# Performance work log

Hardware: AMD Instinct MI355X
Metric: run time of the kernel (lower is better)

The kernel has to match this reference:

```python
import jax, jax.numpy as jnp
import numpy as np

N = 50000
E = 800000
D_IN = 128
D_HID = 128
D_OUT = 64
BN_EPS = 1e-5


def setup_inputs() -> dict:
    key = jax.random.key(0)
    ks = jax.random.split(key, 8)
    x = jax.random.normal(ks[0], (N, D_IN), dtype=jnp.float32)
    edge_index = jax.random.randint(ks[1], (2, E), 0, N, dtype=jnp.int64)
    # fc1
    W1 = jax.random.normal(ks[2], (D_IN, D_HID), dtype=jnp.float32) / np.sqrt(D_IN)
    b1 = jnp.zeros((D_HID,), dtype=jnp.float32)
    # bn1 affine params
    gamma = jnp.ones((D_HID,), dtype=jnp.float32)
    beta = jnp.zeros((D_HID,), dtype=jnp.float32)
    # fc2
    W2 = jax.random.normal(ks[3], (D_HID, D_OUT), dtype=jnp.float32) / np.sqrt(D_HID)
    b2 = jnp.zeros((D_OUT,), dtype=jnp.float32)
    return {"x": x, "W1": W1, "b1": b1, "gamma": gamma, "beta": beta,
            "W2": W2, "b2": b2, "edge_index": edge_index}


def _propagate(x, row, col):
    # add self loops for every node (reference convention)
    n = x.shape[0]
    sl = jnp.arange(n, dtype=row.dtype)
    row_f = jnp.concatenate([row, sl])
    col_f = jnp.concatenate([col, sl])
    # symmetric degree normalization: deg computed over destinations (col)
    deg = jax.ops.segment_sum(jnp.ones_like(col_f, dtype=x.dtype), col_f, num_segments=n)
    dis = deg ** -0.5
    w = dis[col_f] * dis[row_f]                       # [E+N]
    msg = w[:, None] * x[row_f]                       # [E+N, D] gather + scale
    return jax.ops.segment_sum(msg, col_f, num_segments=n)  # scatter-add


def reference(x, W1, b1, gamma, beta, W2, b2, edge_index):
    row, col = edge_index[0], edge_index[1]
    h = x @ W1 + b1                                   # [N, D_HID]
    h = _propagate(h, row, col)
    # BatchNorm1d with batch statistics (training-mode math, deterministic)
    mu = jnp.mean(h, axis=0)
    var = jnp.var(h, axis=0)
    h = (h - mu) * jax.lax.rsqrt(var + BN_EPS) * gamma + beta
    h = jax.nn.relu(h)
    # dropout treated as identity (eval) for a deterministic reference
    h = h @ W2 + b2                                   # [N, D_OUT]
    h = _propagate(h, row, col)
    return jax.nn.log_softmax(h, axis=1)
```

## Files before the change

### kernel.cpp

```cpp
#include <hip/hip_runtime.h>
#include <hip/hip_bf16.h>

#define N_NODES 50000
#define NE      800000
#define DIN     128
#define DHID    128
#define DOUT    64
#define BN_EPS  1e-5f
#define SLOT    64
#define NBUK    196
#define BCAP    4864
#define EPB     2048
#define NPART   32
#define LDW     132
#define LDW2    132
#define G1_BLOCKS ((N_NODES + 63) / 64)

typedef __hip_bfloat16 bf16;
typedef short bf16x8 __attribute__((ext_vector_type(8)));
typedef float f32x4 __attribute__((ext_vector_type(4)));

__device__ __forceinline__ float ldf(const void* p, int i, int isbf) {
    if (isbf) return __bfloat162float(((const bf16*)p)[i]);
    return ((const float*)p)[i];
}
__device__ __forceinline__ unsigned short f2b(float f) {
    bf16 h = __float2bfloat16(f);
    return *(unsigned short*)&h;
}
__device__ __forceinline__ float2 up2(unsigned int u) {
    return make_float2(__uint_as_float(u << 16), __uint_as_float(u & 0xffff0000u));
}
__device__ __forceinline__ unsigned int pk2(float a, float b) {
    return ((unsigned int)f2b(a)) | (((unsigned int)f2b(b)) << 16);
}

#define DETECT_ISBF(W1raw, tid, sdet, isbf_out)                                   \
    if ((tid) == 0) sdet = 0;                                                     \
    __syncthreads();                                                              \
    {                                                                             \
        unsigned int u_ = ((unsigned int)((const unsigned short*)(W1raw))[tid]) << 16; \
        float f_ = fabsf(__uint_as_float(u_));                                    \
        if (!isnan(f_) && !isinf(f_) && f_ > 1e4f) atomicOr(&sdet, 1);            \
    }                                                                             \
    __syncthreads();                                                              \
    const int isbf_out = !sdet;

__global__ __launch_bounds__(256) void k_binA(const void* eiraw, int* __restrict__ gcnt,
                                              unsigned int* __restrict__ bpk) {
    __shared__ int hist4[4][256];
    __shared__ int cur4[4][256];
    __shared__ int eofs[256], gbase[256];
    __shared__ int wsum[4];
    __shared__ unsigned int stg[EPB];
    __shared__ int sdet;
    int tid = threadIdx.x;
    int lane = tid & 63;
    int wv = tid >> 6;
    if (tid == 0) sdet = 0;
    #pragma unroll
    for (int w2 = 0; w2 < 4; ++w2) hist4[w2][tid] = 0;
    __syncthreads();
    if (tid < 64 && ((const unsigned int*)eiraw)[2 * tid + 1] != 0u) atomicOr(&sdet, 1);
    __syncthreads();
    const int isll = !sdet;

    int e0 = blockIdx.x * EPB;
    int nE = NE - e0; if (nE > EPB) nE = EPB;
    int r[8], c[8];
    #pragma unroll
    for (int q = 0; q < 8; ++q) {
        int li = q * 256 + tid;
        if (li < nE) {
            int e = e0 + li;
            if (isll) { r[q] = (int)((const long long*)eiraw)[e]; c[q] = (int)((const long long*)eiraw)[NE + e]; }
            else      { r[q] = ((const int*)eiraw)[e];            c[q] = ((const int*)eiraw)[NE + e]; }
            atomicAdd(&hist4[wv][c[q] >> 8], 1);
        } else r[q] = -1;
    }
    __syncthreads();
    int h0 = hist4[0][tid], h1 = hist4[1][tid], h2 = hist4[2][tid], h3 = hist4[3][tid];
    int tot = h0 + h1 + h2 + h3;
    int inc = tot;
    #pragma unroll
    for (int off = 1; off < 64; off <<= 1) {
        int u = __shfl_up(inc, off, 64);
        if (lane >= off) inc += u;
    }
    if (lane == 63) wsum[wv] = inc;
    __syncthreads();
    int woff = 0;
    #pragma unroll
    for (int w2 = 0; w2 < 3; ++w2) if (w2 < wv) woff += wsum[w2];
    int ex = woff + inc - tot;
    eofs[tid] = ex;
    cur4[0][tid] = ex;
    cur4[1][tid] = ex + h0;
    cur4[2][tid] = ex + h0 + h1;
    cur4[3][tid] = ex + h0 + h1 + h2;
    if (tid < NBUK) gbase[tid] = atomicAdd(&gcnt[tid], tot);
    __syncthreads();
    #pragma unroll
    for (int q = 0; q < 8; ++q) {
        if (r[q] >= 0) {
            int b = c[q] >> 8;
            int p = atomicAdd(&cur4[wv][b], 1);
            stg[p] = ((unsigned int)b << 24) | ((unsigned int)(c[q] & 255) << 16) | (unsigned int)r[q];
        }
    }
    __syncthreads();
    for (int i = tid; i < nE; i += 256) {
        unsigned int v = stg[i];
        int b = v >> 24;
        int pos = gbase[b] + (i - eofs[b]);
        if (pos < BCAP) bpk[(size_t)b * BCAP + pos] = v;
    }
}

__global__ __launch_bounds__(256) void k_binB_gemm1(const unsigned int* __restrict__ bpk,
                                                    const int* __restrict__ gcnt,
                                                    int* __restrict__ counts, float* __restrict__ disv,
                                                    int* __restrict__ ej,
                                                    const void* __restrict__ x, const void* __restrict__ W1,
                                                    const void* __restrict__ b1,
                                                    unsigned short* __restrict__ g1) {
    __shared__ __align__(16) char smraw[33792];
    __shared__ int sdet;
    int tid = threadIdx.x;

    if (blockIdx.x < NBUK) {
        int (*cnt4)[256] = (int(*)[256])smraw;
        int (*cur4)[256] = (int(*)[256])(smraw + 4096);
        int* eofs        = (int*)(smraw + 8192);
        int* wsum        = (int*)(smraw + 9216);
        unsigned int* stg = (unsigned int*)(smraw + 9232);

        int b = blockIdx.x;
        int lane = tid & 63;
        int wv = tid >> 6;
        int m = gcnt[b]; if (m > BCAP) m = BCAP;
        #pragma unroll
        for (int w2 = 0; w2 < 4; ++w2) cnt4[w2][tid] = 0;
        __syncthreads();
        const unsigned int* src = bpk + (size_t)b * BCAP;
        for (int i = tid; i < m; i += 256)
            atomicAdd(&cnt4[wv][(src[i] >> 16) & 255], 1);
        __syncthreads();
        int h0 = cnt4[0][tid], h1 = cnt4[1][tid], h2 = cnt4[2][tid], h3 = cnt4[3][tid];
        int hv = h0 + h1 + h2 + h3;
        int inc = hv;
        #pragma unroll
        for (int off = 1; off < 64; off <<= 1) {
            int u = __shfl_up(inc, off, 64);
            if (lane >= off) inc += u;
        }
        if (lane == 63) wsum[wv] = inc;
        __syncthreads();
        int woff = 0;
        #pragma unroll
        for (int w2 = 0; w2 < 3; ++w2) if (w2 < wv) woff += wsum[w2];
        int ex = woff + inc - hv;
        eofs[tid] = ex;
        cur4[0][tid] = ex;
        cur4[1][tid] = ex + h0;
        cur4[2][tid] = ex + h0 + h1;
        cur4[3][tid] = ex + h0 + h1 + h2;
        int c0 = b << 8;
        int cg = c0 + tid;
        if (cg < N_NODES) {
            counts[cg] = hv;
            disv[cg] = rsqrtf((float)(hv + 1));
            int hc = hv < SLOT ? hv : SLOT;
            int hp = (hc + 15) & ~15; if (hp > SLOT) hp = SLOT;
            for (int k = hc; k < hp; ++k) ej[(size_t)cg * SLOT + k] = N_NODES;
        } else if (cg == N_NODES) {
            disv[cg] = 0.f;
        }
        __syncthreads();
        for (int i = tid; i < m; i += 256) {
            unsigned int v = src[i];
            int cl = (v >> 16) & 255;
            int p = atomicAdd(&cur4[wv][cl], 1);
            stg[p] = v & 0x00ffffffu;
        }
        __syncthreads();
        for (int i = tid; i < m; i += 256) {
            unsigned int v = stg[i];
            int cl = v >> 16;
            int k = i - eofs[cl];
            if (k < SLOT) ej[(size_t)(c0 + cl) * SLOT + k] = (int)(v & 0xffffu);
        }
    } else {
        unsigned short* wt = (unsigned short*)smraw;
        DETECT_ISBF(W1, tid, sdet, isbf)

        #pragma unroll 4
        for (int i = 0; i < 64; ++i) {
            int idx = i * 256 + tid;
            int k = idx >> 7, n = idx & 127;
            wt[n * LDW + k] = isbf ? ((const unsigned short*)W1)[idx]
                                   : f2b(((const float*)W1)[idx]);
        }
        __syncthreads();

        int lane = tid & 63;
        int wave = tid >> 6;
        int bid = blockIdx.x - NBUK;
        int m0 = bid * 64 + wave * 16;
        int lm = lane & 15;
        int quad = lane >> 4;

        bf16x8 a[4];
        int arow = m0 + lm;
        int arow_c = arow < N_NODES ? arow : 0;
        if (isbf) {
            const unsigned short* xb = (const unsigned short*)x;
            #pragma unroll
            for (int q = 0; q < 4; ++q)
                a[q] = *(const bf16x8*)(xb + arow_c * DIN + q * 32 + quad * 8);
        } else {
            const float* xf = (const float*)x;
            #pragma unroll
            for (int q = 0; q < 4; ++q) {
                bf16x8 t;
                #pragma unroll
                for (int j = 0; j < 8; ++j)
                    t[j] = (short)f2b(xf[arow_c * DIN + q * 32 + quad * 8 + j]);
                a[q] = t;
            }
        }

        #pragma unroll
        for (int nt = 0; nt < 8; ++nt) {
            int n0 = nt * 16;
            f32x4 acc = {0.f, 0.f, 0.f, 0.f};
            #pragma unroll
            for (int q = 0; q < 4; ++q) {
                bf16x8 b = *(const bf16x8*)(wt + (n0 + lm) * LDW + q * 32 + quad * 8);
                acc = __builtin_amdgcn_mfma_f32_16x16x32_bf16(a[q], b, acc, 0, 0, 0);
            }
            float bias = ldf(b1, n0 + lm, isbf);
            #pragma unroll
            for (int r = 0; r < 4; ++r) {
                int grow = m0 + quad * 4 + r;
                if (grow <= N_NODES) {
                    float val = (grow < N_NODES) ? (acc[r] + bias) : 0.f;
                    g1[grow * DHID + n0 + lm] = f2b(val);
                }
            }
        }
    }
}

__global__ __launch_bounds__(256) void k_prop1(const int* __restrict__ counts, const float* __restrict__ disv,
                                               const int* __restrict__ ej,
                                               const unsigned int* __restrict__ g1p,
                                               unsigned int* __restrict__ agg1p,
                                               float* __restrict__ statsP) {
    __shared__ float sp[1024];
    int tid = threadIdx.x;
    int w = tid >> 6;
    int n = blockIdx.x * 4 + w;
    n = __builtin_amdgcn_readfirstlane(n);
    int lane = tid & 63;
    float ax = 0.f, ay = 0.f;
    if (n < N_NODES) {
        int cnt = counts[n];
        float dv = disv[n];
        int t = cnt < SLOT ? cnt : SLOT;
        int tp = (t + 15) & ~15; if (tp > SLOT) tp = SLOT;
        const int* ejn = ej + (size_t)n * SLOT;
        float2 v = up2(g1p[(size_t)n * 64 + lane]);
        float ax0 = dv * v.x, ay0 = dv * v.y, ax1 = 0.f, ay1 = 0.f;
        float ax2 = 0.f, ay2 = 0.f, ax3 = 0.f, ay3 = 0.f;
        for (int j = 0; j < tp; j += 16) {
            const int4* ej4 = (const int4*)(ejn + j);
            int4 E0 = ej4[0], E1 = ej4[1], E2 = ej4[2], E3 = ej4[3];
            int e[16] = {E0.x, E0.y, E0.z, E0.w, E1.x, E1.y, E1.z, E1.w,
                         E2.x, E2.y, E2.z, E2.w, E3.x, E3.y, E3.z, E3.w};
            unsigned int gg[16];
            float ds[16];
            #pragma unroll
            for (int q = 0; q < 16; ++q) { gg[q] = g1p[(size_t)e[q] * 64 + lane]; ds[q] = disv[e[q]]; }
            #pragma unroll
            for (int q = 0; q < 16; ++q) {
                float2 f = up2(gg[q]);
                if ((q & 3) == 0) { ax0 = fmaf(ds[q], f.x, ax0); ay0 = fmaf(ds[q], f.y, ay0); }
                else if ((q & 3) == 1) { ax1 = fmaf(ds[q], f.x, ax1); ay1 = fmaf(ds[q], f.y, ay1); }
                else if ((q & 3) == 2) { ax2 = fmaf(ds[q], f.x, ax2); ay2 = fmaf(ds[q], f.y, ay2); }
                else { ax3 = fmaf(ds[q], f.x, ax3); ay3 = fmaf(ds[q], f.y, ay3); }
            }
        }
        ax = dv * ((ax0 + ax1) + (ax2 + ax3));
        ay = dv * ((ay0 + ay1) + (ay2 + ay3));
        agg1p[(size_t)n * 64 + lane] = pk2(ax, ay);
    }
    sp[w * 256 + 2 * lane]       = ax;
    sp[w * 256 + 2 * lane + 1]   = ay;
    sp[w * 256 + 128 + 2 * lane] = ax * ax;
    sp[w * 256 + 129 + 2 * lane] = ay * ay;
    __syncthreads();
    float s = sp[tid] + sp[256 + tid] + sp[512 + tid] + sp[768 + tid];
    atomicAdd(&statsP[(blockIdx.x & (NPART - 1)) * 256 + tid], s);
}

__global__ __launch_bounds__(256) void k_gemm2_mfma(const unsigned int* __restrict__ agg1p,
                                                    const float* __restrict__ statsP,
                                                    const void* __restrict__ gamma, const void* __restrict__ beta,
                                                    const void* __restrict__ W2, const void* __restrict__ b2,
                                                    const void* __restrict__ W1, const int* __restrict__ counts,
                                                    unsigned short* __restrict__ g2) {
    __shared__ unsigned short w2t[64 * LDW2];
    __shared__ float sc[128], sh[128], redu[256];
    __shared__ int sdet;
    int tid = threadIdx.x;
    DETECT_ISBF(W1, tid, sdet, isbf)

    #pragma unroll 4
    for (int i = 0; i < 32; ++i) {
        int idx = i * 256 + tid;
        int k = idx >> 6, n = idx & 63;
        w2t[n * LDW2 + k] = isbf ? ((const unsigned short*)W2)[idx]
                                 : f2b(((const float*)W2)[idx]);
    }
    {
        float s = 0.f;
        #pragma unroll
        for (int p = 0; p < NPART; ++p) s += statsP[p * 256 + tid];
        redu[tid] = s;
    }
    __syncthreads();
    if (tid < 128) {
        const float invn = 1.0f / (float)N_NODES;
        float mu = redu[tid] * invn;
        float var = redu[128 + tid] * invn - mu * mu;
        float rs = rsqrtf(var + BN_EPS);
        float g = ldf(gamma, tid, isbf);
        sc[tid] = rs * g;
        sh[tid] = ldf(beta, tid, isbf) - mu * rs * g;
    }
    __syncthreads();

    int lane = tid & 63;
    int wave = tid >> 6;
    int m0 = blockIdx.x * 64 + wave * 16;
    int lm = lane & 15;
    int quad = lane >> 4;

    int arow = m0 + lm;
    int arow_c = arow < N_NODES ? arow : 0;
    bf16x8 a[4];
    #pragma unroll
    for (int q = 0; q < 4; ++q) {
        uint4 gv = *(const uint4*)(agg1p + (size_t)arow_c * 64 + q * 16 + quad * 4);
        int kb = q * 32 + quad * 8;
        float2 f0 = up2(gv.x), f1 = up2(gv.y), f2 = up2(gv.z), f3 = up2(gv.w);
        float e0 = f0.x * sc[kb + 0] + sh[kb + 0];
        float e1 = f0.y * sc[kb + 1] + sh[kb + 1];
        float e2 = f1.x * sc[kb + 2] + sh[kb + 2];
        float e3 = f1.y * sc[kb + 3] + sh[kb + 3];
        float e4 = f2.x * sc[kb + 4] + sh[kb + 4];
        float e5 = f2.y * sc[kb + 5] + sh[kb + 5];
        float e6 = f3.x * sc[kb + 6] + sh[kb + 6];
        float e7 = f3.y * sc[kb + 7] + sh[kb + 7];
        bf16x8 t;
        t[0] = (short)f2b(e0 > 0.f ? e0 : 0.f);
        t[1] = (short)f2b(e1 > 0.f ? e1 : 0.f);
        t[2] = (short)f2b(e2 > 0.f ? e2 : 0.f);
        t[3] = (short)f2b(e3 > 0.f ? e3 : 0.f);
        t[4] = (short)f2b(e4 > 0.f ? e4 : 0.f);
        t[5] = (short)f2b(e5 > 0.f ? e5 : 0.f);
        t[6] = (short)f2b(e6 > 0.f ? e6 : 0.f);
        t[7] = (short)f2b(e7 > 0.f ? e7 : 0.f);
        a[q] = t;
    }

    float dsc[4];
    #pragma unroll
    for (int r = 0; r < 4; ++r) {
        int grow = m0 + quad * 4 + r;
        dsc[r] = (grow < N_NODES) ? rsqrtf((float)(counts[grow] + 1)) : 0.f;
    }

    #pragma unroll
    for (int nt = 0; nt < 4; ++nt) {
        int n0 = nt * 16;
        f32x4 acc = {0.f, 0.f, 0.f, 0.f};
        #pragma unroll
        for (int q = 0; q < 4; ++q) {
            bf16x8 b = *(const bf16x8*)(w2t + (n0 + lm) * LDW2 + q * 32 + quad * 8);
            acc = __builtin_amdgcn_mfma_f32_16x16x32_bf16(a[q], b, acc, 0, 0, 0);
        }
        float bias = ldf(b2, n0 + lm, isbf);
        #pragma unroll
        for (int r = 0; r < 4; ++r) {
            int grow = m0 + quad * 4 + r;
            if (grow <= N_NODES)
                g2[grow * DOUT + n0 + lm] = f2b(dsc[r] * (acc[r] + bias));
        }
    }
}

__global__ __launch_bounds__(256) void k_prop2_lsm(const int* __restrict__ counts, const int* __restrict__ ej,
                                                   const unsigned int* __restrict__ g2p,
                                                   const void* __restrict__ W1, void* __restrict__ out) {
    __shared__ int sdet;
    int tid = threadIdx.x;
    DETECT_ISBF(W1, tid, sdet, isbf)

    int n = blockIdx.x * 8 + (tid >> 5);
    if (n >= N_NODES) return;
    int lane = tid & 31;
    int cnt = counts[n];
    int t = cnt < SLOT ? cnt : SLOT;
    int tp = (t + 15) & ~15; if (tp > SLOT) tp = SLOT;
    const int* ejn = ej + (size_t)n * SLOT;
    float2 v = up2(g2p[(size_t)n * 32 + lane]);
    float ax0 = v.x, ay0 = v.y, ax1 = 0.f, ay1 = 0.f;
    float ax2 = 0.f, ay2 = 0.f, ax3 = 0.f, ay3 = 0.f;
    for (int j = 0; j < tp; j += 16) {
        const int4* ej4 = (const int4*)(ejn + j);
        int4 E0 = ej4[0], E1 = ej4[1], E2 = ej4[2], E3 = ej4[3];
        int e[16] = {E0.x, E0.y, E0.z, E0.w, E1.x, E1.y, E1.z, E1.w,
                     E2.x, E2.y, E2.z, E2.w, E3.x, E3.y, E3.z, E3.w};
        unsigned int gg[16];
        #pragma unroll
        for (int q = 0; q < 16; ++q) gg[q] = g2p[(size_t)e[q] * 32 + lane];
        #pragma unroll
        for (int q = 0; q < 16; ++q) {
            float2 f = up2(gg[q]);
            if ((q & 3) == 0) { ax0 += f.x; ay0 += f.y; }
            else if ((q & 3) == 1) { ax1 += f.x; ay1 += f.y; }
            else if ((q & 3) == 2) { ax2 += f.x; ay2 += f.y; }
            else { ax3 += f.x; ay3 += f.y; }
        }
    }
    float dv = rsqrtf((float)(cnt + 1));
    float ax = dv * ((ax0 + ax1) + (ax2 + ax3));
    float ay = dv * ((ay0 + ay1) + (ay2 + ay3));
    float m = fmaxf(ax, ay);
    #pragma unroll
    for (int off = 16; off >= 1; off >>= 1) m = fmaxf(m, __shfl_xor(m, off, 32));
    float sum = __expf(ax - m) + __expf(ay - m);
    #pragma unroll
    for (int off = 16; off >= 1; off >>= 1) sum += __shfl_xor(sum, off, 32);
    float lse = m + __logf(sum);
    float rx = ax - lse, ry = ay - lse;
    if (isbf) {
        ((unsigned int*)out)[(size_t)n * 32 + lane] = pk2(rx, ry);
    } else {
        float2* o = (float2*)((float*)out + (size_t)n * 64 + 2 * lane);
        *o = make_float2(rx, ry);
    }
}

extern "C" void kernel_launch(void* const* d_in, const int* in_sizes, int n_in,
                              void* d_out, int out_size, void* d_ws, size_t ws_size,
                              hipStream_t stream) {
    const void* x     = d_in[0];
    const void* W1    = d_in[1];
    const void* b1    = d_in[2];
    const void* gamma = d_in[3];
    const void* beta  = d_in[4];
    const void* W2    = d_in[5];
    const void* b2    = d_in[6];
    const void* ei    = d_in[7];

    char* w = (char*)d_ws;
    float*          statsP = (float*)(w + 0);
    int*            gcnt   = (int*)(w + 32768);
    int*            counts = (int*)(w + 33792);
    float*          disv   = (float*)(w + 233792);
    int*            ej     = (int*)(w + 433808);
    unsigned int*   bpk    = (unsigned int*)(w + 13233808);
    unsigned short* g1     = (unsigned short*)(w + 17047184);
    unsigned int*   agg1p  = (unsigned int*)(w + 29847440);
    unsigned short* g2     = (unsigned short*)(w + 42647440);

    hipMemsetAsync(w, 0, 33792, stream);

    k_binA<<<(NE + EPB - 1) / EPB, 256, 0, stream>>>(ei, gcnt, bpk);

    k_binB_gemm1<<<NBUK + G1_BLOCKS, 256, 0, stream>>>(bpk, gcnt, counts, disv, ej, x, W1, b1, g1);

    k_prop1<<<(N_NODES + 3) / 4, 256, 0, stream>>>(counts, disv, ej, (const unsigned int*)g1, agg1p, statsP);

    k_gemm2_mfma<<<(N_NODES + 63) / 64, 256, 0, stream>>>(agg1p, statsP, gamma, beta, W2, b2,
                                                          W1, counts, g2);

    k_prop2_lsm<<<(N_NODES + 7) / 8, 256, 0, stream>>>(counts, ej, (const unsigned int*)g2, W1, d_out);
}
```

Measured before the change: 213.8 us.

## Split fused bin/GEMM1 kernel into separate launches and register-cache bucket entries

Splits the combined bucket-sort and first-GEMM kernel into two separate kernels, k_binB and k_gemm1_mfma, launched back to back. The bucket kernel now loads its entries into registers once (BREG=19 per thread) instead of reading global memory twice. The GEMM kernel loads bf16 W1 with vectorized 16-byte loads. The split removes the shared-memory sizing compromise and block-type divergence, at the cost of an extra launch and losing the overlap between binning and GEMM.

```diff
diff --git a/kernel.cpp b/kernel.cpp
--- a/kernel.cpp
+++ b/kernel.cpp
@@ -10,11 +10,11 @@
 #define SLOT    64
 #define NBUK    196
 #define BCAP    4864
+#define BREG    19
 #define EPB     2048
 #define NPART   32
 #define LDW     132
 #define LDW2    132
-#define G1_BLOCKS ((N_NODES + 63) / 64)
 
 typedef __hip_bfloat16 bf16;
 typedef short bf16x8 __attribute__((ext_vector_type(8)));
@@ -117,136 +117,155 @@
     }
 }
 
-__global__ __launch_bounds__(256) void k_binB_gemm1(const unsigned int* __restrict__ bpk,
-                                                    const int* __restrict__ gcnt,
-                                                    int* __restrict__ counts, float* __restrict__ disv,
-                                                    int* __restrict__ ej,
-                                                    const void* __restrict__ x, const void* __restrict__ W1,
+__global__ __launch_bounds__(256) void k_binB(const unsigned int* __restrict__ bpk, const int* __restrict__ gcnt,
+                                              int* __restrict__ counts, float* __restrict__ disv,
+                                              int* __restrict__ ej) {
+    __shared__ int cnt4[4][256];
+    __shared__ int cur4[4][256];
+    __shared__ int eofs[256];
+    __shared__ int wsum[4];
+    __shared__ unsigned int stg[BCAP];
+    int b = blockIdx.x;
+    int tid = threadIdx.x;
+    int lane = tid & 63;
+    int wv = tid >> 6;
+    int m = gcnt[b]; if (m > BCAP) m = BCAP;
+    #pragma unroll
+    for (int w2 = 0; w2 < 4; ++w2) cnt4[w2][tid] = 0;
+    __syncthreads();
+    const unsigned int* src = bpk + (size_t)b * BCAP;
+    unsigned int vv[BREG];
+    #pragma unroll
+    for (int q = 0; q < BREG; ++q) {
+        int i = q * 256 + tid;
+        vv[q] = (i < m) ? src[i] : 0xffffffffu;
+        if (vv[q] != 0xffffffffu) atomicAdd(&cnt4[wv][(vv[q] >> 16) & 255], 1);
+    }
+    __syncthreads();
+    int h0 = cnt4[0][tid], h1 = cnt4[1][tid], h2 = cnt4[2][tid], h3 = cnt4[3][tid];
+    int hv = h0 + h1 + h2 + h3;
+    int inc = hv;
+    #pragma unroll
+    for (int off = 1; off < 64; off <<= 1) {
+        int u = __shfl_up(inc, off, 64);
+        if (lane >= off) inc += u;
+    }
+    if (lane == 63) wsum[wv] = inc;
+    __syncthreads();
+    int woff = 0;
+    #pragma unroll
+    for (int w2 = 0; w2 < 3; ++w2) if (w2 < wv) woff += wsum[w2];
+    int ex = woff + inc - hv;
+    eofs[tid] = ex;
+    cur4[0][tid] = ex;
+    cur4[1][tid] = ex + h0;
+    cur4[2][tid] = ex + h0 + h1;
+    cur4[3][tid] = ex + h0 + h1 + h2;
+    int c0 = b << 8;
+    int cg = c0 + tid;
+    if (cg < N_NODES) {
+        counts[cg] = hv;
+        disv[cg] = rsqrtf((float)(hv + 1));
+        int hc = hv < SLOT ? hv : SLOT;
+        int hp = (hc + 15) & ~15; if (hp > SLOT) hp = SLOT;
+        for (int k = hc; k < hp; ++k) ej[(size_t)cg * SLOT + k] = N_NODES;
+    } else if (cg == N_NODES) {
+        disv[cg] = 0.f;
+    }
+    __syncthreads();
+    #pragma unroll
+    for (int q = 0; q < BREG; ++q) {
+        if (vv[q] != 0xffffffffu) {
+            int cl = (vv[q] >> 16) & 255;
+            int p = atomicAdd(&cur4[wv][cl], 1);
+            stg[p] = vv[q] & 0x00ffffffu;
+        }
+    }
+    __syncthreads();
+    for (int i = tid; i < m; i += 256) {
+        unsigned int v = stg[i];
+        int cl = v >> 16;
+        int k = i - eofs[cl];
+        if (k < SLOT) ej[(size_t)(c0 + cl) * SLOT + k] = (int)(v & 0xffffu);
+    }
+}
+
+__global__ __launch_bounds__(256) void k_gemm1_mfma(const void* __restrict__ x, const void* __restrict__ W1,
                                                     const void* __restrict__ b1,
                                                     unsigned short* __restrict__ g1) {
-    __shared__ __align__(16) char smraw[33792];
+    __shared__ unsigned short wt[128 * LDW];
     __shared__ int sdet;
     int tid = threadIdx.x;
-
-    if (blockIdx.x < NBUK) {
-        int (*cnt4)[256] = (int(*)[256])smraw;
-        int (*cur4)[256] = (int(*)[256])(smraw + 4096);
-        int* eofs        = (int*)(smraw + 8192);
-        int* wsum        = (int*)(smraw + 9216);
-        unsigned int* stg = (unsigned int*)(smraw + 9232);
-
-        int b = blockIdx.x;
-        int lane = tid & 63;
-        int wv = tid >> 6;
-        int m = gcnt[b]; if (m > BCAP) m = BCAP;
-        #pragma unroll
-        for (int w2 = 0; w2 < 4; ++w2) cnt4[w2][tid] = 0;
-        __syncthreads();
-        const unsigned int* src = bpk + (size_t)b * BCAP;
-        for (int i = tid; i < m; i += 256)
-            atomicAdd(&cnt4[wv][(src[i] >> 16) & 255], 1);
-        __syncthreads();
-        int h0 = cnt4[0][tid], h1 = cnt4[1][tid], h2 = cnt4[2][tid], h3 = cnt4[3][tid];
-        int hv = h0 + h1 + h2 + h3;
-        int inc = hv;
-        #pragma unroll
-        for (int off = 1; off < 64; off <<= 1) {
-            int u = __shfl_up(inc, off, 64);
-            if (lane >= off) inc += u;
-        }
-        if (lane == 63) wsum[wv] = inc;
-        __syncthreads();
-        int woff = 0;
-        #pragma unroll
-        for (int w2 = 0; w2 < 3; ++w2) if (w2 < wv) woff += wsum[w2];
-        int ex = woff + inc - hv;
-        eofs[tid] = ex;
-        cur4[0][tid] = ex;
-        cur4[1][tid] = ex + h0;
-        cur4[2][tid] = ex + h0 + h1;
-        cur4[3][tid] = ex + h0 + h1 + h2;
-        int c0 = b << 8;
-        int cg = c0 + tid;
-        if (cg < N_NODES) {
-            counts[cg] = hv;
-            disv[cg] = rsqrtf((float)(hv + 1));
-            int hc = hv < SLOT ? hv : SLOT;
-            int hp = (hc + 15) & ~15; if (hp > SLOT) hp = SLOT;
-            for (int k = hc; k < hp; ++k) ej[(size_t)cg * SLOT + k] = N_NODES;
-        } else if (cg == N_NODES) {
-            disv[cg] = 0.f;
-        }
-        __syncthreads();
-        for (int i = tid; i < m; i += 256) {
-            unsigned int v = src[i];
-            int cl = (v >> 16) & 255;
-            int p = atomicAdd(&cur4[wv][cl], 1);
-            stg[p] = v & 0x00ffffffu;
-        }
-        __syncthreads();
-        for (int i = tid; i < m; i += 256) {
-            unsigned int v = stg[i];
-            int cl = v >> 16;
-            int k = i - eofs[cl];
-            if (k < SLOT) ej[(size_t)(c0 + cl) * SLOT + k] = (int)(v & 0xffffu);
+    DETECT_ISBF(W1, tid, sdet, isbf)
+
+    if (isbf) {
+        const unsigned short* wsrc = (const unsigned short*)W1;
+        #pragma unroll
+        for (int i = 0; i < 8; ++i) {
+            int flat = i * 2048 + tid * 8;
+            int k = flat >> 7, n = flat & 127;
+            uint4 v = *(const uint4*)(wsrc + flat);
+            wt[(n + 0) * LDW + k] = (unsigned short)(v.x & 0xffff);
+            wt[(n + 1) * LDW + k] = (unsigned short)(v.x >> 16);
+            wt[(n + 2) * LDW + k] = (unsigned short)(v.y & 0xffff);
+            wt[(n + 3) * LDW + k] = (unsigned short)(v.y >> 16);
+            wt[(n + 4) * LDW + k] = (unsigned short)(v.z & 0xffff);
+            wt[(n + 5) * LDW + k] = (unsigned short)(v.z >> 16);
+            wt[(n + 6) * LDW + k] = (unsigned short)(v.w & 0xffff);
+            wt[(n + 7) * LDW + k] = (unsigned short)(v.w >> 16);
         }
     } else {
-        unsigned short* wt = (unsigned short*)smraw;
-        DETECT_ISBF(W1, tid, sdet, isbf)
-
         #pragma unroll 4
         for (int i = 0; i < 64; ++i) {
             int idx = i * 256 + tid;
             int k = idx >> 7, n = idx & 127;
-            wt[n * LDW + k] = isbf ? ((const unsigned short*)W1)[idx]
-                                   : f2b(((const float*)W1)[idx]);
-        }
-        __syncthreads();
-
-        int lane = tid & 63;
-        int wave = tid >> 6;
-        int bid = blockIdx.x - NBUK;
-        int m0 = bid * 64 + wave * 16;
-        int lm = lane & 15;
-        int quad = lane >> 4;
-
-        bf16x8 a[4];
-        int arow = m0 + lm;
-        int arow_c = arow < N_NODES ? arow : 0;
-        if (isbf) {
-            const unsigned short* xb = (const unsigned short*)x;
+            wt[n * LDW + k] = f2b(((const float*)W1)[idx]);
+        }
+    }
+    __syncthreads();
+
+    int lane = tid & 63;
+    int wave = tid >> 6;
+    int m0 = blockIdx.x * 64 + wave * 16;
+    int lm = lane & 15;
+    int quad = lane >> 4;
+
+    bf16x8 a[4];
+    int arow = m0 + lm;
+    int arow_c = arow < N_NODES ? arow : 0;
+    if (isbf) {
+        const unsigned short* xb = (const unsigned short*)x;
+        #pragma unroll
+        for (int q = 0; q < 4; ++q)
+            a[q] = *(const bf16x8*)(xb + arow_c * DIN + q * 32 + quad * 8);
+    } else {
+        const float* xf = (const float*)x;
+        #pragma unroll
+        for (int q = 0; q < 4; ++q) {
+            bf16x8 t;
             #pragma unroll
-            for (int q = 0; q < 4; ++q)
-                a[q] = *(const bf16x8*)(xb + arow_c * DIN + q * 32 + quad * 8);
-        } else {
-            const float* xf = (const float*)x;
-            #pragma unroll
-            for (int q = 0; q < 4; ++q) {
-                bf16x8 t;
-                #pragma unroll
-                for (int j = 0; j < 8; ++j)
-                    t[j] = (short)f2b(xf[arow_c * DIN + q * 32 + quad * 8 + j]);
-                a[q] = t;
-            }
-        }
-
-        #pragma unroll
-        for (int nt = 0; nt < 8; ++nt) {
-            int n0 = nt * 16;
-            f32x4 acc = {0.f, 0.f, 0.f, 0.f};
-            #pragma unroll
-            for (int q = 0; q < 4; ++q) {
-                bf16x8 b = *(const bf16x8*)(wt + (n0 + lm) * LDW + q * 32 + quad * 8);
-                acc = __builtin_amdgcn_mfma_f32_16x16x32_bf16(a[q], b, acc, 0, 0, 0);
-            }
-            float bias = ldf(b1, n0 + lm, isbf);
-            #pragma unroll
-            for (int r = 0; r < 4; ++r) {
-                int grow = m0 + quad * 4 + r;
-                if (grow <= N_NODES) {
-                    float val = (grow < N_NODES) ? (acc[r] + bias) : 0.f;
-                    g1[grow * DHID + n0 + lm] = f2b(val);
-                }
+            for (int j = 0; j < 8; ++j)
+                t[j] = (short)f2b(xf[arow_c * DIN + q * 32 + quad * 8 + j]);
+            a[q] = t;
+        }
+    }
+
+    #pragma unroll
+    for (int nt = 0; nt < 8; ++nt) {
+        int n0 = nt * 16;
+        f32x4 acc = {0.f, 0.f, 0.f, 0.f};
+        #pragma unroll
+        for (int q = 0; q < 4; ++q) {
+            bf16x8 b = *(const bf16x8*)(wt + (n0 + lm) * LDW + q * 32 + quad * 8);
+            acc = __builtin_amdgcn_mfma_f32_16x16x32_bf16(a[q], b, acc, 0, 0, 0);
+        }
+        float bias = ldf(b1, n0 + lm, isbf);
+        #pragma unroll
+        for (int r = 0; r < 4; ++r) {
+            int grow = m0 + quad * 4 + r;
+            if (grow <= N_NODES) {
+                float val = (grow < N_NODES) ? (acc[r] + bias) : 0.f;
+                g1[grow * DHID + n0 + lm] = f2b(val);
             }
         }
     }
@@ -481,7 +500,9 @@
 
     k_binA<<<(NE + EPB - 1) / EPB, 256, 0, stream>>>(ei, gcnt, bpk);
 
-    k_binB_gemm1<<<NBUK + G1_BLOCKS, 256, 0, stream>>>(bpk, gcnt, counts, disv, ej, x, W1, b1, g1);
+    k_binB<<<NBUK, 256, 0, stream>>>(bpk, gcnt, counts, disv, ej);
+
+    k_gemm1_mfma<<<(N_NODES + 63) / 64, 256, 0, stream>>>(x, W1, b1, g1);
 
     k_prop1<<<(N_NODES + 3) / 4, 256, 0, stream>>>(counts, disv, ej, (const unsigned int*)g1, agg1p, statsP);
 
```

New measurement: 206.8 us, median of 2. 1.03x faster.
